# Performance work log

Measured on AMD Instinct MI355X. Metric: run time of the kernel, lower is better.

Reference implementation:

```python
import jax, jax.numpy as jnp
import numpy as np

B, N, C = 8, 8192, 64
NPOINT = 2048
RADIUS = 0.2
NSAMPLE = 32


def _fps_single(xyz, npoint):
    # xyz: (N, 3). Iterative farthest point sampling, start at index 0.
    n = xyz.shape[0]

    def body(carry, _):
        min_d, last = carry
        d = jnp.sum((xyz - xyz[last]) ** 2, axis=-1)   # (N,)
        min_d = jnp.minimum(min_d, d)
        nxt = jnp.argmax(min_d).astype(jnp.int32)
        return (min_d, nxt), nxt

    init = (jnp.full((n,), jnp.inf, xyz.dtype), jnp.int32(0))
    _, idx = jax.lax.scan(body, init, None, length=npoint - 1)
    return jnp.concatenate([jnp.zeros((1,), jnp.int32), idx])  # (npoint,)


def _ball_query(xyz, new_xyz, radius, nsample):
    # xyz: (B, N, 3), new_xyz: (B, S, 3) -> neighbor idx (B, S, nsample)
    n = xyz.shape[1]
    # squared pairwise distances (B, S, N)
    d2 = (jnp.sum(new_xyz ** 2, -1)[:, :, None]
          + jnp.sum(xyz ** 2, -1)[:, None, :]
          - 2.0 * jnp.einsum('bsc,bnc->bsn', new_xyz, xyz))
    mask = d2 < radius * radius
    # valid indices first, in original order; invalid -> sentinel n
    key = jnp.where(mask, jnp.arange(n, dtype=jnp.int32)[None, None, :], n)
    srt = jnp.sort(key, axis=-1)[:, :, :nsample]      # (B, S, nsample)
    first = srt[:, :, :1]                             # pad with first valid (query itself)
    return jnp.where(srt >= n, first, srt).astype(jnp.int32)


def setup_inputs() -> dict:
    key = jax.random.key(0)
    k = jax.random.split(key, 8)
    s1 = 1.0 / np.sqrt(67.0)
    s2 = 1.0 / np.sqrt(64.0)
    return {
        'xyz': jax.random.uniform(k[0], (B, N, 3), jnp.float32),
        'features': jax.random.normal(k[1], (B, C, N), jnp.float32),
        'W1': jax.random.normal(k[2], (67, 64), jnp.float32) * s1,
        'b1': jnp.zeros((64,), jnp.float32),
        'W2': jax.random.normal(k[3], (64, 64), jnp.float32) * s2,
        'b2': jnp.zeros((64,), jnp.float32),
        'W3': jax.random.normal(k[4], (64, 128), jnp.float32) * s2,
        'b3': jnp.zeros((128,), jnp.float32),
    }


def reference(xyz, features, W1, b1, W2, b2, W3, b3):
    # 1) farthest point sampling -> centroid indices (B, S)
    fps_idx = jax.vmap(_fps_single, in_axes=(0, None))(xyz, NPOINT)
    new_xyz = jnp.take_along_axis(xyz, fps_idx[:, :, None], axis=1)  # (B, S, 3)

    # 2) ball query grouping
    idx = _ball_query(xyz, new_xyz, RADIUS, NSAMPLE)                 # (B, S, K)
    grouped_xyz = jnp.take_along_axis(
        xyz[:, None, :, :], idx[:, :, :, None], axis=2)              # (B, S, K, 3)
    grouped_xyz = grouped_xyz - new_xyz[:, :, None, :]               # relative coords
    feats_n = jnp.transpose(features, (0, 2, 1))                     # (B, N, C)
    grouped_feats = jnp.take_along_axis(
        feats_n[:, None, :, :], idx[:, :, :, None], axis=2)          # (B, S, K, C)
    g = jnp.concatenate([grouped_xyz, grouped_feats], axis=-1)       # (B, S, K, 3+C)

    # 3) shared MLP (1x1 conv2d equivalent) + ReLU
    h = jax.nn.relu(jnp.einsum('bskc,cd->bskd', g, W1) + b1)
    h = jax.nn.relu(jnp.einsum('bskc,cd->bskd', h, W2) + b2)
    h = jax.nn.relu(jnp.einsum('bskc,cd->bskd', h, W3) + b3)         # (B, S, K, 128)

    # 4) max-pool over the neighbor axis
    new_features = jnp.max(h, axis=2)                                # (B, S, 128)
    new_features = jnp.transpose(new_features, (0, 2, 1))            # (B, 128, S)
    return new_xyz, new_features
```

## Files before the change

kernel.cpp:

```cpp
#include <hip/hip_runtime.h>
#include <cstddef>

#define BATCH 8
#define NPTS 8192
#define NFEAT 64
#define NPOINT 2048
#define NSAMPLE 32

__device__ __forceinline__ float sq_nc(float a) {
    float r = a * a;
    asm volatile("" : "+v"(r));
    return r;
}
__device__ __forceinline__ float mul_nc(float a, float b) {
    float r = a * b;
    asm volatile("" : "+v"(r));
    return r;
}

template <int CTRL>
__device__ __forceinline__ float dppmax(float v) {
    int r = __builtin_amdgcn_mov_dpp(__float_as_int(v), CTRL, 0xF, 0xF, true);
    return fmaxf(v, __int_as_float(r));
}

__global__ __launch_bounds__(512) void fps_f1_kernel(const float* __restrict__ xyz,
                                                     const float* __restrict__ features,
                                                     const float* __restrict__ W1,
                                                     float* __restrict__ F1,
                                                     float* __restrict__ newxyz) {
    extern __shared__ float lds[];
    const int tid = threadIdx.x;

    if (blockIdx.x >= 8) {
        const int lane = tid & 63;
        const int chunk = (tid >> 6) & 3;
        const int sub = tid >> 8;
        const int fblk = blockIdx.x - 8;
        const int b = fblk >> 6;
        const int n = ((fblk & 63) << 7) + (sub << 6) + lane;
        const float* fb = features + (size_t)b * NFEAT * NPTS + n;
        const float* wbase = W1 + 3 * 64 + chunk * 16;

        float acc[16];
#pragma unroll
        for (int i = 0; i < 16; ++i) acc[i] = 0.0f;

#pragma unroll 4
        for (int cp = 0; cp < 64; ++cp) {
            float f = fb[(size_t)cp * NPTS];
            const float4* w = reinterpret_cast<const float4*>(wbase + (size_t)cp * 64);
#pragma unroll
            for (int c4 = 0; c4 < 4; ++c4) {
                float4 ww = w[c4];
                acc[c4 * 4 + 0] += f * ww.x;
                acc[c4 * 4 + 1] += f * ww.y;
                acc[c4 * 4 + 2] += f * ww.z;
                acc[c4 * 4 + 3] += f * ww.w;
            }
        }
        float* o = F1 + ((size_t)b * NPTS + n) * 64 + chunk * 16;
#pragma unroll
        for (int c4 = 0; c4 < 4; ++c4) {
            float4 v;
            v.x = acc[c4 * 4 + 0]; v.y = acc[c4 * 4 + 1];
            v.z = acc[c4 * 4 + 2]; v.w = acc[c4 * 4 + 3];
            *reinterpret_cast<float4*>(o + c4 * 4) = v;
        }
        return;
    }

    float* sx = lds;
    float* sy = lds + NPTS;
    float* sz = lds + 2 * NPTS;
    __shared__ alignas(16) unsigned long long redp[2][8];

    const int b = blockIdx.x;
    const int lane = tid & 63;
    const int wid = tid >> 6;
    const float* xb = xyz + (size_t)b * NPTS * 3;

    for (int i = tid; i < NPTS; i += 512) {
        sx[i] = xb[i * 3 + 0];
        sy[i] = xb[i * 3 + 1];
        sz[i] = xb[i * 3 + 2];
    }
    __syncthreads();

    float mx[16], my_[16], mz[16], md[16];
    const int base = tid * 16;
#pragma unroll
    for (int j = 0; j < 16; ++j) {
        mx[j] = sx[base + j];
        my_[j] = sy[base + j];
        mz[j] = sz[base + j];
        md[j] = INFINITY;
    }

    if (tid == 0) {
        newxyz[(size_t)b * NPOINT * 3 + 0] = sx[0];
        newxyz[(size_t)b * NPOINT * 3 + 1] = sy[0];
        newxyz[(size_t)b * NPOINT * 3 + 2] = sz[0];
    }
    float xl = sx[0], yl = sy[0], zl = sz[0];
    int par = 0;

    for (int it = 1; it < NPOINT; ++it) {
        float bv = -1.0f;
        int bi = 0;
#pragma unroll
        for (int j = 0; j < 16; ++j) {
            float dx = mx[j] - xl;
            float dy = my_[j] - yl;
            float dz = mz[j] - zl;
            float d = (sq_nc(dx) + sq_nc(dy)) + sq_nc(dz);
            float m = fminf(md[j], d);
            md[j] = m;
            if (m > bv) { bv = m; bi = base + j; }
        }

        float wv = bv;
        wv = dppmax<0xB1>(wv);
        wv = dppmax<0x4E>(wv);
        wv = dppmax<0x141>(wv);
        wv = dppmax<0x140>(wv);
        wv = dppmax<0x142>(wv);
        wv = dppmax<0x143>(wv);
        float wvf = __int_as_float(__builtin_amdgcn_readlane(__float_as_int(wv), 63));

        unsigned long long msk = __ballot(bv == wvf);
        int src = __builtin_ctzll(msk);
        if (lane == src)
            redp[par][wid] = ((unsigned long long)__float_as_uint(wvf) << 32) |
                             (unsigned int)(~(unsigned int)bi);
        __syncthreads();

        const ulonglong2* rp = (const ulonglong2*)redp[par];
        ulonglong2 r0 = rp[0], r1 = rp[1], r2 = rp[2], r3 = rp[3];
        unsigned long long m0 = (r0.x > r0.y) ? r0.x : r0.y;
        unsigned long long m1 = (r1.x > r1.y) ? r1.x : r1.y;
        unsigned long long m2 = (r2.x > r2.y) ? r2.x : r2.y;
        unsigned long long m3 = (r3.x > r3.y) ? r3.x : r3.y;
        m0 = (m1 > m0) ? m1 : m0;
        m2 = (m3 > m2) ? m3 : m2;
        m0 = (m2 > m0) ? m2 : m0;
        const int fi = (int)(~(unsigned int)m0);

        xl = sx[fi]; yl = sy[fi]; zl = sz[fi];
        if (tid == 0) {
            size_t o = (size_t)b * NPOINT * 3 + (size_t)it * 3;
            newxyz[o + 0] = xl;
            newxyz[o + 1] = yl;
            newxyz[o + 2] = zl;
        }
        par ^= 1;
    }
}

__global__ __launch_bounds__(64) void ball_kernel(const float* __restrict__ xyz,
                                                  const float* __restrict__ newxyz,
                                                  int* __restrict__ ballidx) {
    extern __shared__ float4 s4[];
    const int b = blockIdx.y;
    const int s = blockIdx.x * 64 + threadIdx.x;
    const float* xb = xyz + (size_t)b * NPTS * 3;
    for (int i = threadIdx.x; i < NPTS; i += 64) {
        float x = xb[i * 3 + 0], y = xb[i * 3 + 1], z = xb[i * 3 + 2];
        float sq = (sq_nc(x) + sq_nc(y)) + sq_nc(z);
        s4[i] = make_float4(x, y, z, sq);
    }
    __syncthreads();

    const int sIdx = b * NPOINT + s;
    float cx = newxyz[(size_t)sIdx * 3 + 0];
    float cy = newxyz[(size_t)sIdx * 3 + 1];
    float cz = newxyz[(size_t)sIdx * 3 + 2];
    float cq = (sq_nc(cx) + sq_nc(cy)) + sq_nc(cz);

    int* ob = ballidx + (size_t)sIdx * NSAMPLE;
    int cnt = 0;
    int first = 0;
#pragma unroll 4
    for (int n = 0; n < NPTS; ++n) {
        float4 p = s4[n];
        float dot = __fmaf_rn(cz, p.z, __fmaf_rn(cy, p.y, __fmul_rn(cx, p.x)));
        float d2 = (cq + p.w) - mul_nc(2.0f, dot);
        if (d2 < 0.04f && cnt < NSAMPLE) {
            ob[cnt] = n;
            if (cnt == 0) first = n;
            ++cnt;
        }
    }
    for (int j = cnt; j < NSAMPLE; ++j) ob[j] = first;
}

__global__ __launch_bounds__(256) void mlp_kernel(const float* __restrict__ xyz,
                                                  const float* __restrict__ W1,
                                                  const float* __restrict__ b1,
                                                  const float* __restrict__ W2,
                                                  const float* __restrict__ b2,
                                                  const float* __restrict__ W3,
                                                  const float* __restrict__ b3,
                                                  const float* __restrict__ F1,
                                                  const int* __restrict__ ballidx,
                                                  const float* __restrict__ newxyz,
                                                  float* __restrict__ outF) {
    __shared__ float hbuf[64][256];
    const int tid = threadIdx.x;
    const int k = tid & 31;
    const int sIdx = blockIdx.x * 8 + (tid >> 5);
    const int b = sIdx >> 11;
    const int s = sIdx & (NPOINT - 1);

    const int p = ballidx[(size_t)sIdx * NSAMPLE + k];
    const float* xb = xyz + (size_t)b * NPTS * 3;
    float rx = xb[p * 3 + 0] - newxyz[(size_t)sIdx * 3 + 0];
    float ry = xb[p * 3 + 1] - newxyz[(size_t)sIdx * 3 + 1];
    float rz = xb[p * 3 + 2] - newxyz[(size_t)sIdx * 3 + 2];

    const float* f1p = F1 + ((size_t)b * NPTS + p) * 64;
#pragma unroll 4
    for (int c4 = 0; c4 < 16; ++c4) {
        float4 f  = *reinterpret_cast<const float4*>(f1p + c4 * 4);
        float4 wx = *reinterpret_cast<const float4*>(W1 + c4 * 4);
        float4 wy = *reinterpret_cast<const float4*>(W1 + 64 + c4 * 4);
        float4 wz = *reinterpret_cast<const float4*>(W1 + 128 + c4 * 4);
        float4 bb = *reinterpret_cast<const float4*>(b1 + c4 * 4);
        hbuf[c4 * 4 + 0][tid] = fmaxf(bb.x + f.x + rx * wx.x + ry * wy.x + rz * wz.x, 0.0f);
        hbuf[c4 * 4 + 1][tid] = fmaxf(bb.y + f.y + rx * wx.y + ry * wy.y + rz * wz.y, 0.0f);
        hbuf[c4 * 4 + 2][tid] = fmaxf(bb.z + f.z + rx * wx.z + ry * wy.z + rz * wz.z, 0.0f);
        hbuf[c4 * 4 + 3][tid] = fmaxf(bb.w + f.w + rx * wx.w + ry * wy.w + rz * wz.w, 0.0f);
    }

    float h2[64];
#pragma unroll
    for (int d4 = 0; d4 < 16; ++d4) {
        float4 bb = *reinterpret_cast<const float4*>(b2 + d4 * 4);
        h2[d4 * 4 + 0] = bb.x; h2[d4 * 4 + 1] = bb.y;
        h2[d4 * 4 + 2] = bb.z; h2[d4 * 4 + 3] = bb.w;
    }
#pragma unroll 4
    for (int c = 0; c < 64; ++c) {
        float a = hbuf[c][tid];
        const float4* w = reinterpret_cast<const float4*>(W2 + (size_t)c * 64);
#pragma unroll
        for (int d4 = 0; d4 < 16; ++d4) {
            float4 ww = w[d4];
            h2[d4 * 4 + 0] += a * ww.x;
            h2[d4 * 4 + 1] += a * ww.y;
            h2[d4 * 4 + 2] += a * ww.z;
            h2[d4 * 4 + 3] += a * ww.w;
        }
    }
#pragma unroll
    for (int d = 0; d < 64; ++d) hbuf[d][tid] = fmaxf(h2[d], 0.0f);

    const size_t obase = (size_t)b * 128 * NPOINT + s;
#pragma unroll 1
    for (int ch = 0; ch < 4; ++ch) {
        float acc[32];
#pragma unroll
        for (int j4 = 0; j4 < 8; ++j4) {
            float4 bb = *reinterpret_cast<const float4*>(b3 + ch * 32 + j4 * 4);
            acc[j4 * 4 + 0] = bb.x; acc[j4 * 4 + 1] = bb.y;
            acc[j4 * 4 + 2] = bb.z; acc[j4 * 4 + 3] = bb.w;
        }
#pragma unroll 4
        for (int c = 0; c < 64; ++c) {
            float a = hbuf[c][tid];
            const float4* w = reinterpret_cast<const float4*>(W3 + (size_t)c * 128 + ch * 32);
#pragma unroll
            for (int j4 = 0; j4 < 8; ++j4) {
                float4 ww = w[j4];
                acc[j4 * 4 + 0] += a * ww.x;
                acc[j4 * 4 + 1] += a * ww.y;
                acc[j4 * 4 + 2] += a * ww.z;
                acc[j4 * 4 + 3] += a * ww.w;
            }
        }
#pragma unroll
        for (int j = 0; j < 32; ++j) {
            float v = fmaxf(acc[j], 0.0f);
#pragma unroll
            for (int m = 16; m >= 1; m >>= 1) v = fmaxf(v, __shfl_xor(v, m, 64));
            acc[j] = v;
        }
        if (k == 0) {
#pragma unroll
            for (int j = 0; j < 32; ++j)
                outF[obase + (size_t)(ch * 32 + j) * NPOINT] = acc[j];
        }
    }
}

extern "C" void kernel_launch(void* const* d_in, const int* in_sizes, int n_in,
                              void* d_out, int out_size, void* d_ws, size_t ws_size,
                              hipStream_t stream) {
    const float* xyz      = (const float*)d_in[0];
    const float* features = (const float*)d_in[1];
    const float* W1       = (const float*)d_in[2];
    const float* b1       = (const float*)d_in[3];
    const float* W2       = (const float*)d_in[4];
    const float* b2       = (const float*)d_in[5];
    const float* W3       = (const float*)d_in[6];
    const float* b3       = (const float*)d_in[7];

    float* out_newxyz = (float*)d_out;
    float* out_feat   = (float*)d_out + (size_t)BATCH * NPOINT * 3;

    int*   ballidx = (int*)d_ws;
    float* F1      = (float*)((char*)d_ws + (size_t)BATCH * NPOINT * NSAMPLE * 4);

    fps_f1_kernel<<<8 + 512, 512, 3 * NPTS * 4, stream>>>(xyz, features, W1, F1, out_newxyz);

    ball_kernel<<<dim3(NPOINT / 64, BATCH), 64, NPTS * 16, stream>>>(xyz, out_newxyz, ballidx);

    mlp_kernel<<<(BATCH * NPOINT) / 8, 256, 0, stream>>>(
        xyz, W1, b1, W2, b2, W3, b3, F1, ballidx, out_newxyz, out_feat);
}
```

Measured before the change: 2.514 ms.

## Stage MLP weights in shared memory and keep activations in registers

Measured after the change: 2.649 ms. 1.05x slower.

```diff
diff --git a/kernel.cpp b/kernel.cpp
--- a/kernel.cpp
+++ b/kernel.cpp
@@ -194,55 +194,69 @@
     for (int j = cnt; j < NSAMPLE; ++j) ob[j] = first;
 }
 
-__global__ __launch_bounds__(256) void mlp_kernel(const float* __restrict__ xyz,
-                                                  const float* __restrict__ W1,
-                                                  const float* __restrict__ b1,
-                                                  const float* __restrict__ W2,
-                                                  const float* __restrict__ b2,
-                                                  const float* __restrict__ W3,
-                                                  const float* __restrict__ b3,
-                                                  const float* __restrict__ F1,
-                                                  const int* __restrict__ ballidx,
-                                                  const float* __restrict__ newxyz,
-                                                  float* __restrict__ outF) {
-    __shared__ float hbuf[64][256];
+__global__ __launch_bounds__(256, 3) void mlp_kernel(const float* __restrict__ xyz,
+                                                     const float* __restrict__ W1,
+                                                     const float* __restrict__ b1,
+                                                     const float* __restrict__ W2,
+                                                     const float* __restrict__ b2,
+                                                     const float* __restrict__ W3,
+                                                     const float* __restrict__ b3,
+                                                     const float* __restrict__ F1,
+                                                     const int* __restrict__ ballidx,
+                                                     const float* __restrict__ newxyz,
+                                                     float* __restrict__ outF) {
+    __shared__ float w2s[4096];
+    __shared__ float w3s[8192];
+    __shared__ float w1s[192];
+    __shared__ float b1s[64], b2s[64], b3s[128];
+
     const int tid = threadIdx.x;
     const int k = tid & 31;
     const int sIdx = blockIdx.x * 8 + (tid >> 5);
     const int b = sIdx >> 11;
     const int s = sIdx & (NPOINT - 1);
 
+    for (int i = tid; i < 1024; i += 256)
+        reinterpret_cast<float4*>(w2s)[i] = reinterpret_cast<const float4*>(W2)[i];
+    for (int i = tid; i < 2048; i += 256)
+        reinterpret_cast<float4*>(w3s)[i] = reinterpret_cast<const float4*>(W3)[i];
+    if (tid < 192) w1s[tid] = W1[tid];
+    if (tid < 64)  { b1s[tid] = b1[tid]; b2s[tid] = b2[tid]; }
+    if (tid < 128) b3s[tid] = b3[tid];
+
     const int p = ballidx[(size_t)sIdx * NSAMPLE + k];
     const float* xb = xyz + (size_t)b * NPTS * 3;
     float rx = xb[p * 3 + 0] - newxyz[(size_t)sIdx * 3 + 0];
     float ry = xb[p * 3 + 1] - newxyz[(size_t)sIdx * 3 + 1];
     float rz = xb[p * 3 + 2] - newxyz[(size_t)sIdx * 3 + 2];
-
+    __syncthreads();
+
+    float h1[64];
     const float* f1p = F1 + ((size_t)b * NPTS + p) * 64;
 #pragma unroll 4
     for (int c4 = 0; c4 < 16; ++c4) {
         float4 f  = *reinterpret_cast<const float4*>(f1p + c4 * 4);
-        float4 wx = *reinterpret_cast<const float4*>(W1 + c4 * 4);
-        float4 wy = *reinterpret_cast<const float4*>(W1 + 64 + c4 * 4);
-        float4 wz = *reinterpret_cast<const float4*>(W1 + 128 + c4 * 4);
-        float4 bb = *reinterpret_cast<const float4*>(b1 + c4 * 4);
-        hbuf[c4 * 4 + 0][tid] = fmaxf(bb.x + f.x + rx * wx.x + ry * wy.x + rz * wz.x, 0.0f);
-        hbuf[c4 * 4 + 1][tid] = fmaxf(bb.y + f.y + rx * wx.y + ry * wy.y + rz * wz.y, 0.0f);
-        hbuf[c4 * 4 + 2][tid] = fmaxf(bb.z + f.z + rx * wx.z + ry * wy.z + rz * wz.z, 0.0f);
-        hbuf[c4 * 4 + 3][tid] = fmaxf(bb.w + f.w + rx * wx.w + ry * wy.w + rz * wz.w, 0.0f);
+        float4 wx = *reinterpret_cast<const float4*>(w1s + c4 * 4);
+        float4 wy = *reinterpret_cast<const float4*>(w1s + 64 + c4 * 4);
+        float4 wz = *reinterpret_cast<const float4*>(w1s + 128 + c4 * 4);
+        float4 bb = *reinterpret_cast<const float4*>(b1s + c4 * 4);
+        h1[c4 * 4 + 0] = fmaxf(bb.x + f.x + rx * wx.x + ry * wy.x + rz * wz.x, 0.0f);
+        h1[c4 * 4 + 1] = fmaxf(bb.y + f.y + rx * wx.y + ry * wy.y + rz * wz.y, 0.0f);
+        h1[c4 * 4 + 2] = fmaxf(bb.z + f.z + rx * wx.z + ry * wy.z + rz * wz.z, 0.0f);
+        h1[c4 * 4 + 3] = fmaxf(bb.w + f.w + rx * wx.w + ry * wy.w + rz * wz.w, 0.0f);
     }
 
     float h2[64];
 #pragma unroll
     for (int d4 = 0; d4 < 16; ++d4) {
-        float4 bb = *reinterpret_cast<const float4*>(b2 + d4 * 4);
+        float4 bb = *reinterpret_cast<const float4*>(b2s + d4 * 4);
         h2[d4 * 4 + 0] = bb.x; h2[d4 * 4 + 1] = bb.y;
         h2[d4 * 4 + 2] = bb.z; h2[d4 * 4 + 3] = bb.w;
     }
 #pragma unroll 4
     for (int c = 0; c < 64; ++c) {
-        float a = hbuf[c][tid];
-        const float4* w = reinterpret_cast<const float4*>(W2 + (size_t)c * 64);
+        float a = h1[c];
+        const float4* w = reinterpret_cast<const float4*>(w2s + c * 64);
 #pragma unroll
         for (int d4 = 0; d4 < 16; ++d4) {
             float4 ww = w[d4];
@@ -253,7 +267,7 @@
         }
     }
 #pragma unroll
-    for (int d = 0; d < 64; ++d) hbuf[d][tid] = fmaxf(h2[d], 0.0f);
+    for (int d = 0; d < 64; ++d) h2[d] = fmaxf(h2[d], 0.0f);
 
     const size_t obase = (size_t)b * 128 * NPOINT + s;
 #pragma unroll 1
@@ -261,14 +275,14 @@
         float acc[32];
 #pragma unroll
         for (int j4 = 0; j4 < 8; ++j4) {
-            float4 bb = *reinterpret_cast<const float4*>(b3 + ch * 32 + j4 * 4);
+            float4 bb = *reinterpret_cast<const float4*>(b3s + ch * 32 + j4 * 4);
             acc[j4 * 4 + 0] = bb.x; acc[j4 * 4 + 1] = bb.y;
             acc[j4 * 4 + 2] = bb.z; acc[j4 * 4 + 3] = bb.w;
         }
 #pragma unroll 4
         for (int c = 0; c < 64; ++c) {
-            float a = hbuf[c][tid];
-            const float4* w = reinterpret_cast<const float4*>(W3 + (size_t)c * 128 + ch * 32);
+            float a = h2[c];
+            const float4* w = reinterpret_cast<const float4*>(w3s + c * 128 + ch * 32);
 #pragma unroll
             for (int j4 = 0; j4 < 8; ++j4) {
                 float4 ww = w[j4];
```
